# Kernel optimization log

Hardware: AMD Instinct MI355X
Metric: run time of the kernel (lower is better)

The kernel has to match this reference:

```python
import jax, jax.numpy as jnp
import numpy as np

N_HEAD = 16
ROPE_BASE = 10000.0


def _rope_cos_sin(T, D, dtype):
    # inv_freq over even dims, freqs concatenated twice (rotate_half convention)
    inv_freq = 1.0 / (ROPE_BASE ** (jnp.arange(0, D, 2, dtype=jnp.float32) / D))
    t = jnp.arange(T, dtype=jnp.float32)
    freqs = jnp.outer(t, inv_freq)          # [T, D/2]
    emb = jnp.concatenate([freqs, freqs], axis=-1)  # [T, D]
    return jnp.cos(emb).astype(dtype), jnp.sin(emb).astype(dtype)


def _rotate_half(x):
    x1, x2 = jnp.split(x, 2, axis=-1)
    return jnp.concatenate([-x2, x1], axis=-1)


def setup_inputs() -> dict:
    key = jax.random.key(0)
    ks = jax.random.split(key, 5)
    B, T, C = 2, 2048, 1024
    s = 1.0 / np.sqrt(C)
    return {
        "x": jax.random.normal(ks[0], (B, T, C), jnp.float32),
        "W_attn": jax.random.normal(ks[1], (C, 3 * C), jnp.float32) * s,
        "b_attn": jax.random.normal(ks[2], (3 * C,), jnp.float32) * 0.02,
        "W_proj": jax.random.normal(ks[3], (C, C), jnp.float32) * s,
        "b_proj": jax.random.normal(ks[4], (C,), jnp.float32) * 0.02,
    }


def reference(x, W_attn, b_attn, W_proj, b_proj):
    B, T, C = x.shape
    H = N_HEAD
    D = C // H

    # fused QKV projection
    qkv = x @ W_attn + b_attn                      # [B, T, 3C]
    q, k, v = jnp.split(qkv, 3, axis=-1)
    q = q.reshape(B, T, H, D).transpose(0, 2, 1, 3)  # [B, H, T, D]
    k = k.reshape(B, T, H, D).transpose(0, 2, 1, 3)
    v = v.reshape(B, T, H, D).transpose(0, 2, 1, 3)

    # RoPE (no past_kv: applied to full q and k)
    cos, sin = _rope_cos_sin(T, D, x.dtype)        # [T, D]
    cos = cos[None, None]                          # [1, 1, T, D]
    sin = sin[None, None]
    q = q * cos + _rotate_half(q) * sin
    k = k * cos + _rotate_half(k) * sin

    # causal SDPA (dropout_p = 0 in reference)
    scale = 1.0 / np.sqrt(D)
    scores = jnp.einsum("bhqd,bhkd->bhqk", q, k) * scale
    causal = jnp.tril(jnp.ones((T, T), dtype=bool))
    scores = jnp.where(causal, scores, jnp.finfo(scores.dtype).min)
    attn = jax.nn.softmax(scores, axis=-1)
    y = jnp.einsum("bhqk,bhkd->bhqd", attn, v)     # [B, H, T, D]

    y = y.transpose(0, 2, 1, 3).reshape(B, T, C)
    y = y @ W_proj + b_proj
    return y
```

## Files before the change

kernel.cpp:

```cpp
#include <hip/hip_runtime.h>
#include <cstdint>
#include <cstddef>

#define SEQ_T 2048
#define NHEAD 16

typedef __attribute__((ext_vector_type(8))) short short8;
typedef __attribute__((ext_vector_type(4))) float f32x4;
typedef __attribute__((ext_vector_type(16))) float f32x16;

__device__ __forceinline__ unsigned short f2bf(float f) {
  union { float f; unsigned int u; } v; v.f = f;
  return (unsigned short)((v.u + 0x7FFFu + ((v.u >> 16) & 1u)) >> 16);
}

__device__ __forceinline__ unsigned cvtpk(float lo, float hi) {
  unsigned r;
  asm("v_cvt_pk_bf16_f32 %0, %1, %2" : "=v"(r) : "v"(lo), "v"(hi));
  return r;
}

#if __has_builtin(__builtin_amdgcn_permlane32_swap)
__device__ __forceinline__ void plswap(unsigned& a, unsigned& b) {
  auto r = __builtin_amdgcn_permlane32_swap(a, b, false, false);
  a = r[0];
  b = r[1];
}
#else
__device__ __forceinline__ void plswap(unsigned& a, unsigned& b) {
  asm volatile("s_nop 1\n\tv_permlane32_swap_b32 %0, %1\n\ts_nop 1"
               : "+v"(a), "+v"(b));
}
#endif

__device__ __forceinline__ float xhalf_max(float x) {
  unsigned a = __builtin_bit_cast(unsigned, x), b = a;
  plswap(a, b);
  return fmaxf(__builtin_bit_cast(float, a), __builtin_bit_cast(float, b));
}
__device__ __forceinline__ float xhalf_add(float x) {
  unsigned a = __builtin_bit_cast(unsigned, x), b = a;
  plswap(a, b);
  return __builtin_bit_cast(float, a) + __builtin_bit_cast(float, b);
}

__device__ __forceinline__ float vmax16(const f32x16 v) {
  float a0 = fmaxf(v[0], v[8]),  a1 = fmaxf(v[1], v[9]);
  float a2 = fmaxf(v[2], v[10]), a3 = fmaxf(v[3], v[11]);
  float a4 = fmaxf(v[4], v[12]), a5 = fmaxf(v[5], v[13]);
  float a6 = fmaxf(v[6], v[14]), a7 = fmaxf(v[7], v[15]);
  float b0 = fmaxf(a0, a4), b1 = fmaxf(a1, a5);
  float b2 = fmaxf(a2, a6), b3 = fmaxf(a3, a7);
  return fmaxf(fmaxf(b0, b1), fmaxf(b2, b3));
}

__device__ __forceinline__ void gl_lds16(const void* g, void* l) {
  __builtin_amdgcn_global_load_lds(
      (__attribute__((address_space(1))) void*)(void*)g,
      (__attribute__((address_space(3))) void*)l, 16, 0, 0);
}

__global__ void k_cvt(const float* __restrict__ in, unsigned short* __restrict__ out, int n4) {
  int i = blockIdx.x * 256 + threadIdx.x;
  if (i >= n4) return;
  float4 v = ((const float4*)in)[i];
  unsigned long long pk = (unsigned long long)f2bf(v.x)
                        | ((unsigned long long)f2bf(v.y) << 16)
                        | ((unsigned long long)f2bf(v.z) << 32)
                        | ((unsigned long long)f2bf(v.w) << 48);
  ((unsigned long long*)out)[i] = pk;
}

__global__ void k_tr(const float* __restrict__ in, unsigned short* __restrict__ out, int K, int N) {
  int idx = blockIdx.x * 256 + threadIdx.x;
  int n = idx % N;
  int k0 = (idx / N) * 8;
  short8 v;
#pragma unroll
  for (int j = 0; j < 8; ++j)
    v[j] = (short)f2bf(in[(size_t)(k0 + j) * N + n]);
  *(short8*)&out[(size_t)n * K + k0] = v;
}

__global__ void k_tab(float2* __restrict__ tab) {
  int idx = blockIdx.x * 256 + threadIdx.x;
  int t = idx >> 5, i = idx & 31;
  float inv = powf(10000.0f, -(float)(2 * i) / 64.0f);
  float f = (float)t * inv;
  tab[idx] = make_float2(cosf(f), sinf(f));
}

__global__ void k_gemm_qkv(const unsigned short* __restrict__ A,
                           const unsigned short* __restrict__ Bt,
                           const float* __restrict__ bias,
                           const float2* __restrict__ cs,
                           unsigned short* __restrict__ qo,
                           unsigned short* __restrict__ ko,
                           unsigned short* __restrict__ vo) {
  __shared__ unsigned short lA[128 * 32];
  __shared__ unsigned short lB[128 * 32];
  const int K = 1024;
  const int bn = blockIdx.x, bm = blockIdx.y;
  const int tid = threadIdx.x, w = tid >> 6, l = tid & 63;
  const int lr = l & 15, lh = l >> 4;
  const int wm = w >> 1, wn = w & 1;

  f32x4 acc[4][4];
#pragma unroll
  for (int m = 0; m < 4; ++m)
#pragma unroll
    for (int n = 0; n < 4; ++n)
#pragma unroll
      for (int i = 0; i < 4; ++i) acc[m][n][i] = 0.f;

  const unsigned short* ga0 = A + (size_t)(bm * 128 + w * 16 + (l >> 2)) * K + (l & 3) * 8;
  const unsigned short* gb0 = Bt + (size_t)(bn * 128 + w * 16 + (l >> 2)) * K + (l & 3) * 8;
  unsigned short* la0 = &lA[w * 512];
  unsigned short* la1 = &lA[(w + 4) * 512];
  unsigned short* lb0 = &lB[w * 512];
  unsigned short* lb1 = &lB[(w + 4) * 512];

  for (int kt = 0; kt < K; kt += 32) {
    gl_lds16(ga0 + kt, la0);
    gl_lds16(ga0 + (size_t)64 * K + kt, la1);
    gl_lds16(gb0 + kt, lb0);
    gl_lds16(gb0 + (size_t)64 * K + kt, lb1);
    __syncthreads();
    short8 af[4], bf[4];
#pragma unroll
    for (int m = 0; m < 4; ++m) af[m] = *(const short8*)&lA[(wm * 64 + m * 16 + lr) * 32 + lh * 8];
#pragma unroll
    for (int n = 0; n < 4; ++n) bf[n] = *(const short8*)&lB[(wn * 64 + n * 16 + lr) * 32 + lh * 8];
#pragma unroll
    for (int m = 0; m < 4; ++m)
#pragma unroll
      for (int n = 0; n < 4; ++n)
        acc[m][n] = __builtin_amdgcn_mfma_f32_16x16x32_bf16(af[m], bf[n], acc[m][n], 0, 0, 0);
    __syncthreads();
  }

  const int col0 = bn * 128 + wn * 64;
  const int row0 = bm * 128 + wm * 64;
  const int sec = col0 >> 10;
  const int hh = (col0 >> 6) & 15;
  float bl[4];
#pragma unroll
  for (int n = 0; n < 4; ++n) bl[n] = bias[col0 + n * 16 + lr];

  if (sec == 2) {
    const int b = row0 >> 11;
    unsigned short* vtp = vo + (size_t)(b * 16 + hh) * 64 * 2048;
#pragma unroll
    for (int n = 0; n < 4; ++n) {
      int d = n * 16 + lr;
#pragma unroll
      for (int m = 0; m < 4; ++m) {
        int t = (row0 + m * 16 + lh * 4) & 2047;
        unsigned long long pk = (unsigned long long)f2bf(acc[m][n][0] + bl[n])
                              | ((unsigned long long)f2bf(acc[m][n][1] + bl[n]) << 16)
                              | ((unsigned long long)f2bf(acc[m][n][2] + bl[n]) << 32)
                              | ((unsigned long long)f2bf(acc[m][n][3] + bl[n]) << 48);
        *(unsigned long long*)&vtp[(size_t)d * 2048 + t] = pk;
      }
    }
  } else {
    unsigned short* dst = (sec == 0) ? qo : ko;
#pragma unroll
    for (int m = 0; m < 4; ++m)
#pragma unroll
      for (int i = 0; i < 4; ++i) {
        int row = row0 + m * 16 + lh * 4 + i;
        int t = row & 2047, b = row >> 11;
        size_t ob = ((size_t)(b * 16 + hh) * 2048 + t) * 64;
#pragma unroll
        for (int n = 0; n < 4; ++n) {
          float v = acc[m][n][i] + bl[n];
          float pv = acc[m][n ^ 2][i] + bl[n ^ 2];
          int d = n * 16 + lr;
          float2 c = cs[t * 32 + (d & 31)];
          float rot = (d < 32) ? -pv : pv;
          dst[ob + d] = f2bf(v * c.x + rot * c.y);
        }
      }
  }
}

__global__ __launch_bounds__(512, 4) void k_attn(const unsigned short* __restrict__ Q,
                       const unsigned short* __restrict__ Kg,
                       const unsigned short* __restrict__ VT,
                       unsigned short* __restrict__ O) {
  __shared__ unsigned short kl[2][128 * 64];
  __shared__ unsigned short vl[2][64 * 128];
  const int id = blockIdx.x;
  const int xcd = id & 7, u = id >> 3;
  const int g = u >> 4;
  const int bh = xcd * 4 + g;
  const int s = (u + g * 4) & 15;
  const int qt = (s & 1) ? 15 - (s >> 1) : (s >> 1);
  const int tid = threadIdx.x, w = tid >> 6, l = tid & 63;
  const int wq = w & 3, wk = w >> 2;
  const int lq = l & 31, hi = l >> 5;
  const size_t base = (size_t)bh * SEQ_T * 64;
  const float CE = 0.18033688f;
  const float DTHR = 44.3614f;

  const int qrow = qt * 128 + wq * 32 + lq;
  short8 qf[4];
#pragma unroll
  for (int c = 0; c < 4; ++c)
    qf[c] = *(const short8*)&Q[base + (size_t)qrow * 64 + c * 16 + hi * 8];

  const int kv0 = tid >> 3;
  const unsigned short* ks0 = Kg + base + (size_t)kv0 * 64 + (((tid & 7) ^ (kv0 & 7)) * 8);
  const int dv0 = tid >> 4;
  const unsigned short* vs0 = VT + base + (size_t)dv0 * 2048 + (((tid & 15) ^ (dv0 & 15)) * 8);

#define STAGE(KT, BSEL) do { \
    const unsigned short* kp_ = ks0 + (size_t)(KT) * 8192; \
    const unsigned short* vp_ = vs0 + (size_t)(KT) * 128;  \
    unsigned short* kd_ = &kl[BSEL][w * 512]; \
    unsigned short* vd_ = &vl[BSEL][w * 512]; \
    gl_lds16(kp_,         kd_);        gl_lds16(kp_ + 4096,  kd_ + 4096); \
    gl_lds16(vp_,         vd_);        gl_lds16(vp_ + 65536, vd_ + 4096); \
  } while (0)

  float mi = -1.0e30f, li = 0.f;
  f32x16 oc0, oc1;
#pragma unroll
  for (int r = 0; r < 16; ++r) { oc0[r] = 0.f; oc1[r] = 0.f; }

  const int nkt = qt + 1;
  STAGE(0, 0);
  __syncthreads();

  for (int kt = 0; kt < nkt; ++kt) {
    const int cur = kt & 1;
    if (kt + 1 < nkt) STAGE(kt + 1, cur ^ 1);
    const unsigned short* kb = &kl[cur][0];
    const unsigned short* vb = &vl[cur][0];

    f32x16 st[2];
#pragma unroll
    for (int tt = 0; tt < 2; ++tt)
#pragma unroll
      for (int r = 0; r < 16; ++r) st[tt][r] = 0.f;

    __builtin_amdgcn_s_setprio(1);
#pragma unroll
    for (int tt = 0; tt < 2; ++tt) {
      const int rowb = (wk * 64 + tt * 32 + lq) * 64;
#pragma unroll
      for (int c = 0; c < 4; ++c) {
        const short8 kf = *(const short8*)&kb[rowb + (((c * 2 + hi) ^ (lq & 7)) * 8)];
        st[tt] = __builtin_amdgcn_mfma_f32_32x32x16_bf16(kf, qf[c], st[tt], 0, 0, 0);
      }
    }
    __builtin_amdgcn_s_setprio(0);

    if (kt == nkt - 1) {
#pragma unroll
      for (int tt = 0; tt < 2; ++tt)
#pragma unroll
        for (int r = 0; r < 16; ++r) {
          int kvg = kt * 128 + wk * 64 + tt * 32 + (r & 3) + 8 * (r >> 2) + 4 * hi;
          if (kvg > qrow) st[tt][r] = -3.0e38f;
        }
    }

    float tm = xhalf_max(fmaxf(vmax16(st[0]), vmax16(st[1])));

    if (!__all(tm <= mi + DTHR)) {
      float mn = fmaxf(mi, tm);
      float scq = exp2f((mi - mn) * CE);
      mi = mn;
      li *= scq;
#pragma unroll
      for (int r = 0; r < 16; ++r) {
        float sc_r = __shfl(scq, (r & 3) + 8 * (r >> 2) + 4 * hi, 64);
        oc0[r] *= sc_r;
        oc1[r] *= sc_r;
      }
    }

    const float nb = mi * CE;
    float rs = 0.f;
#pragma unroll
    for (int tt = 0; tt < 2; ++tt)
#pragma unroll
      for (int r = 0; r < 16; ++r) {
        float p = exp2f(fmaf(st[tt][r], CE, -nb));
        st[tt][r] = p;
        rs += p;
      }
    li += xhalf_add(rs);

    short8 pa[4];
#pragma unroll
    for (int kc = 0; kc < 4; ++kc) {
      const int tt = kc >> 1, o = (kc & 1) * 8;
      unsigned w0 = cvtpk(st[tt][o + 0], st[tt][o + 1]);
      unsigned w1 = cvtpk(st[tt][o + 2], st[tt][o + 3]);
      unsigned w2 = cvtpk(st[tt][o + 4], st[tt][o + 5]);
      unsigned w3 = cvtpk(st[tt][o + 6], st[tt][o + 7]);
      plswap(w0, w2);
      plswap(w1, w3);
      uint4 F;
      F.x = w0; F.y = w1; F.z = w2; F.w = w3;
      pa[kc] = __builtin_bit_cast(short8, F);
    }

    __builtin_amdgcn_s_setprio(1);
#pragma unroll
    for (int kc = 0; kc < 4; ++kc) {
      const int chs = ((wk * 8 + kc * 2 + hi) ^ (lq & 15)) * 8;
      const short8 vb0 = *(const short8*)&vb[lq * 128 + chs];
      oc0 = __builtin_amdgcn_mfma_f32_32x32x16_bf16(pa[kc], vb0, oc0, 0, 0, 0);
      const short8 vb1 = *(const short8*)&vb[(32 + lq) * 128 + chs];
      oc1 = __builtin_amdgcn_mfma_f32_32x32x16_bf16(pa[kc], vb1, oc1, 0, 0, 0);
    }
    __builtin_amdgcn_s_setprio(0);

    if (kt + 1 < nkt) __syncthreads();
  }

  __syncthreads();
  float* obuf = (float*)&kl[0][0];
  float* mlb  = (float*)&vl[0][0];
  if (wk == 1) {
#pragma unroll
    for (int r = 0; r < 16; ++r) {
      const int q = (r & 3) + 8 * (r >> 2) + 4 * hi;
      obuf[wq * 2048 + q * 64 + lq]      = oc0[r];
      obuf[wq * 2048 + q * 64 + 32 + lq] = oc1[r];
    }
    if (hi == 0) {
      mlb[wq * 64 + lq * 2 + 0] = mi;
      mlb[wq * 64 + lq * 2 + 1] = li;
    }
  }
  __syncthreads();
  if (wk == 0) {
    const int hh = bh & 15, bb = bh >> 4;
#pragma unroll
    for (int r = 0; r < 16; ++r) {
      const int q = (r & 3) + 8 * (r >> 2) + 4 * hi;
      float m0 = __shfl(mi, q, 64), l0 = __shfl(li, q, 64);
      float m1 = mlb[wq * 64 + q * 2 + 0], l1 = mlb[wq * 64 + q * 2 + 1];
      float mm = fmaxf(m0, m1);
      float f0 = exp2f((m0 - mm) * CE), f1 = exp2f((m1 - mm) * CE);
      float inv = 1.0f / (f0 * l0 + f1 * l1);
      float o0 = (f0 * oc0[r] + f1 * obuf[wq * 2048 + q * 64 + lq]) * inv;
      float o1 = (f0 * oc1[r] + f1 * obuf[wq * 2048 + q * 64 + 32 + lq]) * inv;
      int qg = qt * 128 + wq * 32 + q;
      size_t ob = (size_t)(bb * 2048 + qg) * 1024 + hh * 64;
      O[ob + lq]      = f2bf(o0);
      O[ob + 32 + lq] = f2bf(o1);
    }
  }
#undef STAGE
}

__global__ void k_gemm_proj(const unsigned short* __restrict__ A,
                            const unsigned short* __restrict__ Bt,
                            const float* __restrict__ bias,
                            float* __restrict__ out) {
  __shared__ unsigned short lA[128 * 32];
  __shared__ unsigned short lB[128 * 32];
  const int K = 1024;
  const int bn = blockIdx.x, bm = blockIdx.y;
  const int tid = threadIdx.x, w = tid >> 6, l = tid & 63;
  const int lr = l & 15, lh = l >> 4;
  const int wm = w >> 1, wn = w & 1;

  f32x4 acc[4][4];
#pragma unroll
  for (int m = 0; m < 4; ++m)
#pragma unroll
    for (int n = 0; n < 4; ++n)
#pragma unroll
      for (int i = 0; i < 4; ++i) acc[m][n][i] = 0.f;

  const unsigned short* ga0 = A + (size_t)(bm * 128 + w * 16 + (l >> 2)) * K + (l & 3) * 8;
  const unsigned short* gb0 = Bt + (size_t)(bn * 128 + w * 16 + (l >> 2)) * K + (l & 3) * 8;
  unsigned short* la0 = &lA[w * 512];
  unsigned short* la1 = &lA[(w + 4) * 512];
  unsigned short* lb0 = &lB[w * 512];
  unsigned short* lb1 = &lB[(w + 4) * 512];

  for (int kt = 0; kt < K; kt += 32) {
    gl_lds16(ga0 + kt, la0);
    gl_lds16(ga0 + (size_t)64 * K + kt, la1);
    gl_lds16(gb0 + kt, lb0);
    gl_lds16(gb0 + (size_t)64 * K + kt, lb1);
    __syncthreads();
    short8 af[4], bf[4];
#pragma unroll
    for (int m = 0; m < 4; ++m) af[m] = *(const short8*)&lA[(wm * 64 + m * 16 + lr) * 32 + lh * 8];
#pragma unroll
    for (int n = 0; n < 4; ++n) bf[n] = *(const short8*)&lB[(wn * 64 + n * 16 + lr) * 32 + lh * 8];
#pragma unroll
    for (int m = 0; m < 4; ++m)
#pragma unroll
      for (int n = 0; n < 4; ++n)
        acc[m][n] = __builtin_amdgcn_mfma_f32_16x16x32_bf16(af[m], bf[n], acc[m][n], 0, 0, 0);
    __syncthreads();
  }

  const int col0 = bn * 128 + wn * 64;
  const int row0 = bm * 128 + wm * 64;
  float bl[4];
#pragma unroll
  for (int n = 0; n < 4; ++n) bl[n] = bias[col0 + n * 16 + lr];
#pragma unroll
  for (int m = 0; m < 4; ++m)
#pragma unroll
    for (int i = 0; i < 4; ++i) {
      int row = row0 + m * 16 + lh * 4 + i;
#pragma unroll
      for (int n = 0; n < 4; ++n)
        out[(size_t)row * 1024 + col0 + n * 16 + lr] = acc[m][n][i] + bl[n];
    }
}

extern "C" void kernel_launch(void* const* d_in, const int* in_sizes, int n_in,
                              void* d_out, int out_size, void* d_ws, size_t ws_size,
                              hipStream_t stream) {
  const float* x     = (const float*)d_in[0];
  const float* Wattn = (const float*)d_in[1];
  const float* battn = (const float*)d_in[2];
  const float* Wproj = (const float*)d_in[3];
  const float* bproj = (const float*)d_in[4];
  float* out = (float*)d_out;

  char* ws = (char*)d_ws;
  unsigned short* xb  = (unsigned short*)(ws);
  unsigned short* wat = (unsigned short*)(ws + (8ull  << 20));
  unsigned short* wpt = (unsigned short*)(ws + (14ull << 20));
  unsigned short* qa  = (unsigned short*)(ws + (16ull << 20));
  unsigned short* ka  = (unsigned short*)(ws + (24ull << 20));
  unsigned short* va  = (unsigned short*)(ws + (32ull << 20));
  unsigned short* ob  = (unsigned short*)(ws + (40ull << 20));
  float2* cs          = (float2*)(ws + (48ull << 20));

  k_cvt<<<(4096 * 1024 / 4) / 256, 256, 0, stream>>>(x, xb, 4096 * 1024 / 4);
  k_tr<<<(3072 * 1024 / 8) / 256, 256, 0, stream>>>(Wattn, wat, 1024, 3072);
  k_tr<<<(1024 * 1024 / 8) / 256, 256, 0, stream>>>(Wproj, wpt, 1024, 1024);
  k_tab<<<(2048 * 32) / 256, 256, 0, stream>>>(cs);
  k_gemm_qkv<<<dim3(24, 32), 256, 0, stream>>>(xb, wat, battn, cs, qa, ka, va);
  k_attn<<<512, 512, 0, stream>>>(qa, ka, va, ob);
  k_gemm_proj<<<dim3(8, 32), 256, 0, stream>>>(ob, wpt, bproj, out);
}
```

Before: 138.8 us.

## Merge prep kernels into one launch and give attention warps two query tiles

The four preprocessing kernels (x conversion, two weight transposes, RoPE table) are folded into a single kernel that branches on block index, saving three launches. The attention kernel drops from 8 to 4 warps per block, and each warp now handles two 32-row query tiles, so every K and V fragment read from LDS feeds twice as many MFMAs. Each thread also issues twice as many global-to-LDS copies per stage. This raises register pressure (doubled Q fragments and accumulators) and the launch bound changes from (512,4) to (256,2), which affects occupancy and latency hiding.

```diff
diff --git a/kernel.cpp b/kernel.cpp
--- a/kernel.cpp
+++ b/kernel.cpp
@@ -60,34 +60,45 @@
       (__attribute__((address_space(3))) void*)l, 16, 0, 0);
 }
 
-__global__ void k_cvt(const float* __restrict__ in, unsigned short* __restrict__ out, int n4) {
-  int i = blockIdx.x * 256 + threadIdx.x;
-  if (i >= n4) return;
-  float4 v = ((const float4*)in)[i];
-  unsigned long long pk = (unsigned long long)f2bf(v.x)
-                        | ((unsigned long long)f2bf(v.y) << 16)
-                        | ((unsigned long long)f2bf(v.z) << 32)
-                        | ((unsigned long long)f2bf(v.w) << 48);
-  ((unsigned long long*)out)[i] = pk;
-}
-
-__global__ void k_tr(const float* __restrict__ in, unsigned short* __restrict__ out, int K, int N) {
-  int idx = blockIdx.x * 256 + threadIdx.x;
-  int n = idx % N;
-  int k0 = (idx / N) * 8;
-  short8 v;
-#pragma unroll
-  for (int j = 0; j < 8; ++j)
-    v[j] = (short)f2bf(in[(size_t)(k0 + j) * N + n]);
-  *(short8*)&out[(size_t)n * K + k0] = v;
-}
-
-__global__ void k_tab(float2* __restrict__ tab) {
-  int idx = blockIdx.x * 256 + threadIdx.x;
-  int t = idx >> 5, i = idx & 31;
-  float inv = powf(10000.0f, -(float)(2 * i) / 64.0f);
-  float f = (float)t * inv;
-  tab[idx] = make_float2(cosf(f), sinf(f));
+__global__ void k_prep(const float* __restrict__ x,
+                       const float* __restrict__ Wa,
+                       const float* __restrict__ Wp,
+                       unsigned short* __restrict__ xb,
+                       unsigned short* __restrict__ wat,
+                       unsigned short* __restrict__ wpt,
+                       float2* __restrict__ tab) {
+  const int b = blockIdx.x, tid = threadIdx.x;
+  if (b < 4096) {
+    int i = b * 256 + tid;
+    float4 v = ((const float4*)x)[i];
+    unsigned long long pk = (unsigned long long)f2bf(v.x)
+                          | ((unsigned long long)f2bf(v.y) << 16)
+                          | ((unsigned long long)f2bf(v.z) << 32)
+                          | ((unsigned long long)f2bf(v.w) << 48);
+    ((unsigned long long*)xb)[i] = pk;
+  } else if (b < 5632) {
+    int idx = (b - 4096) * 256 + tid;
+    int n = idx % 3072, k0 = (idx / 3072) * 8;
+    short8 v;
+#pragma unroll
+    for (int j = 0; j < 8; ++j)
+      v[j] = (short)f2bf(Wa[(size_t)(k0 + j) * 3072 + n]);
+    *(short8*)&wat[(size_t)n * 1024 + k0] = v;
+  } else if (b < 6144) {
+    int idx = (b - 5632) * 256 + tid;
+    int n = idx & 1023, k0 = (idx >> 10) * 8;
+    short8 v;
+#pragma unroll
+    for (int j = 0; j < 8; ++j)
+      v[j] = (short)f2bf(Wp[(size_t)(k0 + j) * 1024 + n]);
+    *(short8*)&wpt[(size_t)n * 1024 + k0] = v;
+  } else {
+    int idx = (b - 6144) * 256 + tid;
+    int t = idx >> 5, i = idx & 31;
+    float inv = powf(10000.0f, -(float)(2 * i) / 64.0f);
+    float f = (float)t * inv;
+    tab[idx] = make_float2(cosf(f), sinf(f));
+  }
 }
 
 __global__ void k_gemm_qkv(const unsigned short* __restrict__ A,
@@ -185,12 +196,11 @@
   }
 }
 
-__global__ __launch_bounds__(512, 4) void k_attn(const unsigned short* __restrict__ Q,
+__global__ __launch_bounds__(256, 2) void k_attn(const unsigned short* __restrict__ Q,
                        const unsigned short* __restrict__ Kg,
                        const unsigned short* __restrict__ VT,
                        unsigned short* __restrict__ O) {
-  __shared__ unsigned short kl[2][128 * 64];
-  __shared__ unsigned short vl[2][64 * 128];
+  __shared__ unsigned short smem[32768];
   const int id = blockIdx.x;
   const int xcd = id & 7, u = id >> 3;
   const int g = u >> 4;
@@ -198,17 +208,21 @@
   const int s = (u + g * 4) & 15;
   const int qt = (s & 1) ? 15 - (s >> 1) : (s >> 1);
   const int tid = threadIdx.x, w = tid >> 6, l = tid & 63;
-  const int wq = w & 3, wk = w >> 2;
+  const int wq = w & 1, wk = w >> 1;
   const int lq = l & 31, hi = l >> 5;
   const size_t base = (size_t)bh * SEQ_T * 64;
   const float CE = 0.18033688f;
   const float DTHR = 44.3614f;
 
-  const int qrow = qt * 128 + wq * 32 + lq;
-  short8 qf[4];
-#pragma unroll
-  for (int c = 0; c < 4; ++c)
-    qf[c] = *(const short8*)&Q[base + (size_t)qrow * 64 + c * 16 + hi * 8];
+  int qrow[2];
+  short8 qf[2][4];
+#pragma unroll
+  for (int ta = 0; ta < 2; ++ta) {
+    qrow[ta] = qt * 128 + wq * 64 + ta * 32 + lq;
+    #pragma unroll
+    for (int c = 0; c < 4; ++c)
+      qf[ta][c] = *(const short8*)&Q[base + (size_t)qrow[ta] * 64 + c * 16 + hi * 8];
+  }
 
   const int kv0 = tid >> 3;
   const unsigned short* ks0 = Kg + base + (size_t)kv0 * 64 + (((tid & 7) ^ (kv0 & 7)) * 8);
@@ -218,16 +232,22 @@
 #define STAGE(KT, BSEL) do { \
     const unsigned short* kp_ = ks0 + (size_t)(KT) * 8192; \
     const unsigned short* vp_ = vs0 + (size_t)(KT) * 128;  \
-    unsigned short* kd_ = &kl[BSEL][w * 512]; \
-    unsigned short* vd_ = &vl[BSEL][w * 512]; \
-    gl_lds16(kp_,         kd_);        gl_lds16(kp_ + 4096,  kd_ + 4096); \
-    gl_lds16(vp_,         vd_);        gl_lds16(vp_ + 65536, vd_ + 4096); \
+    unsigned short* kd_ = &smem[(BSEL) * 8192 + w * 512]; \
+    unsigned short* vd_ = &smem[16384 + (BSEL) * 8192 + w * 512]; \
+    gl_lds16(kp_,         kd_);        gl_lds16(kp_ + 2048,  kd_ + 2048); \
+    gl_lds16(kp_ + 4096,  kd_ + 4096); gl_lds16(kp_ + 6144,  kd_ + 6144); \
+    gl_lds16(vp_,          vd_);        gl_lds16(vp_ + 32768, vd_ + 2048); \
+    gl_lds16(vp_ + 65536,  vd_ + 4096); gl_lds16(vp_ + 98304, vd_ + 6144); \
   } while (0)
 
-  float mi = -1.0e30f, li = 0.f;
-  f32x16 oc0, oc1;
-#pragma unroll
-  for (int r = 0; r < 16; ++r) { oc0[r] = 0.f; oc1[r] = 0.f; }
+  float mi[2] = {-1.0e30f, -1.0e30f}, li[2] = {0.f, 0.f};
+  f32x16 oc[2][2];
+#pragma unroll
+  for (int ta = 0; ta < 2; ++ta)
+#pragma unroll
+    for (int dt = 0; dt < 2; ++dt)
+#pragma unroll
+      for (int r = 0; r < 16; ++r) oc[ta][dt][r] = 0.f;
 
   const int nkt = qt + 1;
   STAGE(0, 0);
@@ -236,126 +256,143 @@
   for (int kt = 0; kt < nkt; ++kt) {
     const int cur = kt & 1;
     if (kt + 1 < nkt) STAGE(kt + 1, cur ^ 1);
-    const unsigned short* kb = &kl[cur][0];
-    const unsigned short* vb = &vl[cur][0];
-
-    f32x16 st[2];
-#pragma unroll
-    for (int tt = 0; tt < 2; ++tt)
-#pragma unroll
-      for (int r = 0; r < 16; ++r) st[tt][r] = 0.f;
-
-    __builtin_amdgcn_s_setprio(1);
-#pragma unroll
-    for (int tt = 0; tt < 2; ++tt) {
-      const int rowb = (wk * 64 + tt * 32 + lq) * 64;
+    const unsigned short* kb = &smem[cur * 8192];
+    const unsigned short* vb = &smem[16384 + cur * 8192];
+    const bool diag = (kt == nkt - 1);
+
+#pragma unroll
+    for (int tk = 0; tk < 2; ++tk) {
+      const int krow = (wk * 64 + tk * 32 + lq) * 64;
+      short8 kf[4];
+#pragma unroll
+      for (int c = 0; c < 4; ++c)
+        kf[c] = *(const short8*)&kb[krow + (((2 * c + hi) ^ (lq & 7)) * 8)];
+
+      f32x16 st[2];
+#pragma unroll
+      for (int ta = 0; ta < 2; ++ta)
+#pragma unroll
+        for (int r = 0; r < 16; ++r) st[ta][r] = 0.f;
+
+      __builtin_amdgcn_s_setprio(1);
 #pragma unroll
       for (int c = 0; c < 4; ++c) {
-        const short8 kf = *(const short8*)&kb[rowb + (((c * 2 + hi) ^ (lq & 7)) * 8)];
-        st[tt] = __builtin_amdgcn_mfma_f32_32x32x16_bf16(kf, qf[c], st[tt], 0, 0, 0);
-      }
+        st[0] = __builtin_amdgcn_mfma_f32_32x32x16_bf16(kf[c], qf[0][c], st[0], 0, 0, 0);
+        st[1] = __builtin_amdgcn_mfma_f32_32x32x16_bf16(kf[c], qf[1][c], st[1], 0, 0, 0);
+      }
+      __builtin_amdgcn_s_setprio(0);
+
+      if (diag) {
+#pragma unroll
+        for (int ta = 0; ta < 2; ++ta)
+#pragma unroll
+          for (int r = 0; r < 16; ++r) {
+            int kvg = kt * 128 + wk * 64 + tk * 32 + (r & 3) + 8 * (r >> 2) + 4 * hi;
+            if (kvg > qrow[ta]) st[ta][r] = -3.0e38f;
+          }
+      }
+
+      short8 pa[2][2];
+#pragma unroll
+      for (int ta = 0; ta < 2; ++ta) {
+        float tm = xhalf_max(vmax16(st[ta]));
+        if (!__all(tm <= mi[ta] + DTHR)) {
+          float mn = fmaxf(mi[ta], tm);
+          float scq = exp2f((mi[ta] - mn) * CE);
+          mi[ta] = mn;
+          li[ta] *= scq;
+#pragma unroll
+          for (int r = 0; r < 16; ++r) {
+            float sc_r = __shfl(scq, (r & 3) + 8 * (r >> 2) + 4 * hi, 64);
+            oc[ta][0][r] *= sc_r;
+            oc[ta][1][r] *= sc_r;
+          }
+        }
+        const float nb = mi[ta] * CE;
+        float rs = 0.f;
+#pragma unroll
+        for (int r = 0; r < 16; ++r) {
+          float p = exp2f(fmaf(st[ta][r], CE, -nb));
+          st[ta][r] = p;
+          rs += p;
+        }
+        li[ta] += xhalf_add(rs);
+#pragma unroll
+        for (int kc = 0; kc < 2; ++kc) {
+          const int o = kc * 8;
+          unsigned w0 = cvtpk(st[ta][o + 0], st[ta][o + 1]);
+          unsigned w1 = cvtpk(st[ta][o + 2], st[ta][o + 3]);
+          unsigned w2 = cvtpk(st[ta][o + 4], st[ta][o + 5]);
+          unsigned w3 = cvtpk(st[ta][o + 6], st[ta][o + 7]);
+          plswap(w0, w2);
+          plswap(w1, w3);
+          uint4 F;
+          F.x = w0; F.y = w1; F.z = w2; F.w = w3;
+          pa[ta][kc] = __builtin_bit_cast(short8, F);
+        }
+      }
+
+      short8 vbf[2][2];
+#pragma unroll
+      for (int dt = 0; dt < 2; ++dt)
+#pragma unroll
+        for (int kc = 0; kc < 2; ++kc)
+          vbf[dt][kc] = *(const short8*)&vb[(dt * 32 + lq) * 128 +
+                          (((wk * 8 + tk * 4 + kc * 2 + hi) ^ (lq & 15)) * 8)];
+
+      __builtin_amdgcn_s_setprio(1);
+#pragma unroll
+      for (int ta = 0; ta < 2; ++ta)
+#pragma unroll
+        for (int dt = 0; dt < 2; ++dt)
+#pragma unroll
+          for (int kc = 0; kc < 2; ++kc)
+            oc[ta][dt] = __builtin_amdgcn_mfma_f32_32x32x16_bf16(pa[ta][kc], vbf[dt][kc], oc[ta][dt], 0, 0, 0);
+      __builtin_amdgcn_s_setprio(0);
     }
-    __builtin_amdgcn_s_setprio(0);
-
-    if (kt == nkt - 1) {
-#pragma unroll
-      for (int tt = 0; tt < 2; ++tt)
-#pragma unroll
-        for (int r = 0; r < 16; ++r) {
-          int kvg = kt * 128 + wk * 64 + tt * 32 + (r & 3) + 8 * (r >> 2) + 4 * hi;
-          if (kvg > qrow) st[tt][r] = -3.0e38f;
-        }
-    }
-
-    float tm = xhalf_max(fmaxf(vmax16(st[0]), vmax16(st[1])));
-
-    if (!__all(tm <= mi + DTHR)) {
-      float mn = fmaxf(mi, tm);
-      float scq = exp2f((mi - mn) * CE);
-      mi = mn;
-      li *= scq;
+
+    if (kt + 1 < nkt) __syncthreads();
+  }
+
+  __syncthreads();
+  float* obuf = (float*)&smem[0];
+  float* mlb  = (float*)&smem[16384];
+  if (wk == 1) {
+#pragma unroll
+    for (int ta = 0; ta < 2; ++ta) {
 #pragma unroll
       for (int r = 0; r < 16; ++r) {
-        float sc_r = __shfl(scq, (r & 3) + 8 * (r >> 2) + 4 * hi, 64);
-        oc0[r] *= sc_r;
-        oc1[r] *= sc_r;
-      }
-    }
-
-    const float nb = mi * CE;
-    float rs = 0.f;
-#pragma unroll
-    for (int tt = 0; tt < 2; ++tt)
-#pragma unroll
-      for (int r = 0; r < 16; ++r) {
-        float p = exp2f(fmaf(st[tt][r], CE, -nb));
-        st[tt][r] = p;
-        rs += p;
-      }
-    li += xhalf_add(rs);
-
-    short8 pa[4];
-#pragma unroll
-    for (int kc = 0; kc < 4; ++kc) {
-      const int tt = kc >> 1, o = (kc & 1) * 8;
-      unsigned w0 = cvtpk(st[tt][o + 0], st[tt][o + 1]);
-      unsigned w1 = cvtpk(st[tt][o + 2], st[tt][o + 3]);
-      unsigned w2 = cvtpk(st[tt][o + 4], st[tt][o + 5]);
-      unsigned w3 = cvtpk(st[tt][o + 6], st[tt][o + 7]);
-      plswap(w0, w2);
-      plswap(w1, w3);
-      uint4 F;
-      F.x = w0; F.y = w1; F.z = w2; F.w = w3;
-      pa[kc] = __builtin_bit_cast(short8, F);
-    }
-
-    __builtin_amdgcn_s_setprio(1);
-#pragma unroll
-    for (int kc = 0; kc < 4; ++kc) {
-      const int chs = ((wk * 8 + kc * 2 + hi) ^ (lq & 15)) * 8;
-      const short8 vb0 = *(const short8*)&vb[lq * 128 + chs];
-      oc0 = __builtin_amdgcn_mfma_f32_32x32x16_bf16(pa[kc], vb0, oc0, 0, 0, 0);
-      const short8 vb1 = *(const short8*)&vb[(32 + lq) * 128 + chs];
-      oc1 = __builtin_amdgcn_mfma_f32_32x32x16_bf16(pa[kc], vb1, oc1, 0, 0, 0);
-    }
-    __builtin_amdgcn_s_setprio(0);
-
-    if (kt + 1 < nkt) __syncthreads();
-  }
-
-  __syncthreads();
-  float* obuf = (float*)&kl[0][0];
-  float* mlb  = (float*)&vl[0][0];
-  if (wk == 1) {
-#pragma unroll
-    for (int r = 0; r < 16; ++r) {
-      const int q = (r & 3) + 8 * (r >> 2) + 4 * hi;
-      obuf[wq * 2048 + q * 64 + lq]      = oc0[r];
-      obuf[wq * 2048 + q * 64 + 32 + lq] = oc1[r];
-    }
-    if (hi == 0) {
-      mlb[wq * 64 + lq * 2 + 0] = mi;
-      mlb[wq * 64 + lq * 2 + 1] = li;
+        const int q = ta * 32 + (r & 3) + 8 * (r >> 2) + 4 * hi;
+        obuf[wq * 4096 + q * 64 + lq]      = oc[ta][0][r];
+        obuf[wq * 4096 + q * 64 + 32 + lq] = oc[ta][1][r];
+      }
+      if (hi == 0) {
+        mlb[wq * 128 + (ta * 32 + lq) * 2 + 0] = mi[ta];
+        mlb[wq * 128 + (ta * 32 + lq) * 2 + 1] = li[ta];
+      }
     }
   }
   __syncthreads();
   if (wk == 0) {
     const int hh = bh & 15, bb = bh >> 4;
 #pragma unroll
-    for (int r = 0; r < 16; ++r) {
-      const int q = (r & 3) + 8 * (r >> 2) + 4 * hi;
-      float m0 = __shfl(mi, q, 64), l0 = __shfl(li, q, 64);
-      float m1 = mlb[wq * 64 + q * 2 + 0], l1 = mlb[wq * 64 + q * 2 + 1];
-      float mm = fmaxf(m0, m1);
-      float f0 = exp2f((m0 - mm) * CE), f1 = exp2f((m1 - mm) * CE);
-      float inv = 1.0f / (f0 * l0 + f1 * l1);
-      float o0 = (f0 * oc0[r] + f1 * obuf[wq * 2048 + q * 64 + lq]) * inv;
-      float o1 = (f0 * oc1[r] + f1 * obuf[wq * 2048 + q * 64 + 32 + lq]) * inv;
-      int qg = qt * 128 + wq * 32 + q;
-      size_t ob = (size_t)(bb * 2048 + qg) * 1024 + hh * 64;
-      O[ob + lq]      = f2bf(o0);
-      O[ob + 32 + lq] = f2bf(o1);
-    }
+    for (int ta = 0; ta < 2; ++ta)
+#pragma unroll
+      for (int r = 0; r < 16; ++r) {
+        const int qloc = (r & 3) + 8 * (r >> 2) + 4 * hi;
+        const int q = ta * 32 + qloc;
+        float m0 = __shfl(mi[ta], qloc, 64), l0 = __shfl(li[ta], qloc, 64);
+        float m1 = mlb[wq * 128 + q * 2 + 0], l1 = mlb[wq * 128 + q * 2 + 1];
+        float mm = fmaxf(m0, m1);
+        float f0 = exp2f((m0 - mm) * CE), f1 = exp2f((m1 - mm) * CE);
+        float inv = 1.0f / (f0 * l0 + f1 * l1);
+        float o0 = (f0 * oc[ta][0][r] + f1 * obuf[wq * 4096 + q * 64 + lq]) * inv;
+        float o1 = (f0 * oc[ta][1][r] + f1 * obuf[wq * 4096 + q * 64 + 32 + lq]) * inv;
+        int qg = qt * 128 + wq * 64 + q;
+        size_t ob = (size_t)(bb * 2048 + qg) * 1024 + hh * 64;
+        O[ob + lq]      = f2bf(o0);
+        O[ob + 32 + lq] = f2bf(o1);
+      }
   }
 #undef STAGE
 }
@@ -442,11 +479,8 @@
   unsigned short* ob  = (unsigned short*)(ws + (40ull << 20));
   float2* cs          = (float2*)(ws + (48ull << 20));
 
-  k_cvt<<<(4096 * 1024 / 4) / 256, 256, 0, stream>>>(x, xb, 4096 * 1024 / 4);
-  k_tr<<<(3072 * 1024 / 8) / 256, 256, 0, stream>>>(Wattn, wat, 1024, 3072);
-  k_tr<<<(1024 * 1024 / 8) / 256, 256, 0, stream>>>(Wproj, wpt, 1024, 1024);
-  k_tab<<<(2048 * 32) / 256, 256, 0, stream>>>(cs);
+  k_prep<<<6400, 256, 0, stream>>>(x, Wattn, Wproj, xb, wat, wpt, cs);
   k_gemm_qkv<<<dim3(24, 32), 256, 0, stream>>>(xb, wat, battn, cs, qa, ka, va);
-  k_attn<<<512, 512, 0, stream>>>(qa, ka, va, ob);
+  k_attn<<<512, 256, 0, stream>>>(qa, ka, va, ob);
   k_gemm_proj<<<dim3(8, 32), 256, 0, stream>>>(ob, wpt, bproj, out);
 }
```

After: 140.0 us. Within noise of the previous version (+0.9%).
